# Performance work log

Hardware: AMD Instinct MI355X
Metric: run time of the kernel (lower is better)

The kernel has to match this reference:

```python
import jax, jax.numpy as jnp
import numpy as np
import math

D_MODEL = 1024
EPS = 1e-6  # RMSNorm epsilon


def setup_inputs() -> dict:
    key = jax.random.key(0)
    ks = jax.random.split(key, 9)
    d = D_MODEL
    B, T = 4, 4096
    s = 1.0 / math.sqrt(d)
    return {
        "x": jax.random.normal(ks[0], (B, T, d), dtype=jnp.float32),
        "w_key": jax.random.normal(ks[1], (2 * d, d), dtype=jnp.float32) * s,  # Linear(d, 2d, bias=False)
        "conv_w": jax.random.normal(ks[2], (d, 1, 3), dtype=jnp.float32) * (1.0 / math.sqrt(3)),  # depthwise k=3
        "conv_b": jax.random.normal(ks[3], (d,), dtype=jnp.float32) * 0.02,
        "w1": jax.random.normal(ks[4], (2 * d, d), dtype=jnp.float32) * s,  # Linear(d, 2d)
        "b1": jax.random.normal(ks[5], (2 * d,), dtype=jnp.float32) * 0.02,
        "w2": jax.random.normal(ks[6], (d, 2 * d), dtype=jnp.float32) * (1.0 / math.sqrt(2 * d)),  # Linear(2d, d)
        "b2": jax.random.normal(ks[7], (d,), dtype=jnp.float32) * 0.02,
        "norm_w": jnp.ones((d,), dtype=jnp.float32),
    }


def parallel_lerp_scan(theta, alpha):
    # h_t = lerp(h_{t-1}, theta_t, alpha_t) = (1-alpha_t)*h_{t-1} + alpha_t*theta_t
    # Linear recurrence h_t = a_t*h_{t-1} + b_t -> log-depth associative scan.
    a = 1.0 - alpha
    b = alpha * theta

    def combine(c1, c2):
        a1, b1 = c1
        a2, b2 = c2
        return (a2 * a1, a2 * b1 + b2)

    _, h = jax.lax.associative_scan(combine, (a, b), axis=1)
    return h


def rms_norm(x, w):
    var = jnp.mean(jnp.square(x), axis=-1, keepdims=True)
    return x * jax.lax.rsqrt(var + EPS) * w


def reference(x, w_key, conv_w, conv_b, w1, b1, w2, b2, norm_w):
    d = x.shape[-1]
    res = jnp.einsum('btd,ed->bte', x, w_key)  # [B,T,2D]
    theta, alpha = res[..., :d], res[..., d:]
    h = parallel_lerp_scan(jnp.tanh(theta) * math.pi, jax.nn.sigmoid(alpha))
    h = h.astype(x.dtype)
    # causal depthwise conv: left-pad (k-1)=2 zeros along time
    h_t = jnp.transpose(h, (0, 2, 1))  # [B,D,T]
    conv = jax.lax.conv_general_dilated(
        h_t, conv_w, window_strides=(1,), padding=[(2, 0)],
        feature_group_count=d, dimension_numbers=('NCH', 'OIH', 'NCH'))
    h_bound = jnp.transpose(conv + conv_b[None, :, None], (0, 2, 1))  # [B,T,D]
    z = h + h_bound
    hid = jax.nn.silu(jnp.einsum('btd,ed->bte', z, w1) + b1)
    h_final = jnp.einsum('bte,de->btd', hid, w2) + b2
    return rms_norm(h_final, norm_w)
```

## Files before the change

### kernel.cpp

```cpp
#include <hip/hip_runtime.h>

typedef unsigned short u16;
typedef unsigned int u32;
typedef __attribute__((ext_vector_type(8))) short short8;
typedef __attribute__((ext_vector_type(4))) float f32x4;

#define T_LEN 4096
#define BATCH 4
#define M_TOT (BATCH*T_LEN)
#define NCHUNK 32
#define CLEN 128

__device__ __forceinline__ u16 f2bf(float f){
  u32 u = __builtin_bit_cast(u32, f);
  u32 r = (u + 0x7FFFu + ((u >> 16) & 1u)) >> 16;
  return (u16)r;
}
__device__ __forceinline__ float sigmoid_(float v){ return 1.f/(1.f + __expf(-v)); }
__device__ __forceinline__ float tanh_pi_(float v){
  return 3.14159265358979323846f * (1.f - 2.f/(1.f + __expf(2.f*v)));
}

__global__ __launch_bounds__(256) void cvt_bf16_k(const float* __restrict__ in,
                                                  u16* __restrict__ out, int n4){
  int g = blockIdx.x*256 + threadIdx.x;
  if (g >= n4) return;
  float4 v = reinterpret_cast<const float4*>(in)[g];
  reinterpret_cast<ushort4*>(out)[g] =
      make_ushort4(f2bf(v.x), f2bf(v.y), f2bf(v.z), f2bf(v.w));
}


#define GBAR() do { __builtin_amdgcn_sched_barrier(0); __builtin_amdgcn_s_barrier(); \
                    __builtin_amdgcn_sched_barrier(0); } while(0)
#define WAITLGKM0() do { asm volatile("s_waitcnt lgkmcnt(0)" ::: "memory"); \
                         __builtin_amdgcn_sched_barrier(0); } while(0)
#define VMCNT(n) do { asm volatile("s_waitcnt vmcnt(" #n ")" ::: "memory"); \
                      __builtin_amdgcn_sched_barrier(0); } while(0)

#define STAGE(buf, ab, q, kt) do { \
  const u16* _s = ((ab) ? Bb : Ab) + (size_t)(q)*rowK64 + (size_t)(kt)*64; \
  __builtin_amdgcn_global_load_lds( \
    (const __attribute__((address_space(1))) void*)_s, \
    (__attribute__((address_space(3))) void*)(smem + (buf)*65536 + (ab)*32768 + (q)*8192 + stb), \
    16, 0, 0); \
} while(0)

#define LDA(buf, m, kk) (*(const short8*)(smem + (buf)*65536 + aRow + (m)*2048 + ((kk) ? csw1 : csw0)))
#define LDB(buf, n, kk) (*(const short8*)(smem + (buf)*65536 + 32768 + bRow + (n)*2048 + ((kk) ? csw1 : csw0)))

#define LOADB(buf) do { _Pragma("unroll") for (int n=0;n<4;n++){ \
    bfr0[n] = LDB(buf,n,0); bfr1[n] = LDB(buf,n,1); } } while(0)

#define PHASE_Q(buf, q, STMTS, ENDSTMT) do { \
  short8 _a00 = LDA(buf, 2*(q)  , 0); \
  short8 _a01 = LDA(buf, 2*(q)  , 1); \
  short8 _a10 = LDA(buf, 2*(q)+1, 0); \
  short8 _a11 = LDA(buf, 2*(q)+1, 1); \
  STMTS \
  GBAR(); \
  WAITLGKM0(); \
  __builtin_amdgcn_s_setprio(1); \
  _Pragma("unroll") \
  for (int n=0;n<4;n++){ \
    acc[2*(q)][n]   = __builtin_amdgcn_mfma_f32_16x16x32_bf16(_a00, bfr0[n], acc[2*(q)][n], 0,0,0); \
    acc[2*(q)][n]   = __builtin_amdgcn_mfma_f32_16x16x32_bf16(_a01, bfr1[n], acc[2*(q)][n], 0,0,0); \
    acc[2*(q)+1][n] = __builtin_amdgcn_mfma_f32_16x16x32_bf16(_a10, bfr0[n], acc[2*(q)+1][n], 0,0,0); \
    acc[2*(q)+1][n] = __builtin_amdgcn_mfma_f32_16x16x32_bf16(_a11, bfr1[n], acc[2*(q)+1][n], 0,0,0); \
  } \
  __builtin_amdgcn_s_setprio(0); \
  ENDSTMT \
  GBAR(); \
} while(0)

template<int EPI>
__global__ __launch_bounds__(512, 2) void gemm8p(
    const u16* __restrict__ Ag, const u16* __restrict__ Bg,
    const float* __restrict__ bias, void* __restrict__ Cout,
    int M, int N, int K)
{
  extern __shared__ __attribute__((aligned(16))) char smem[];
  const int tid = threadIdx.x;
  const int wid = tid >> 6, lane = tid & 63;
  const int wr = wid >> 2, wc = wid & 3;
  const int fr = lane & 15, fq = lane >> 4;

  const int nbn = N >> 8;
  const int nwg = gridDim.x;
  const int bid = blockIdx.x;
  const int swzb = (bid & 7) * (nwg >> 3) + (bid >> 3);
  const int bm = swzb / nbn, bn = swzb - bm * nbn;

  const size_t rowK64 = (size_t)64 * K;
  const u16* Ab = Ag + ((size_t)bm*256 + (tid>>3)) * K + ((tid & 7) ^ ((tid >> 3) & 7)) * 8;
  const u16* Bb = Bg + ((size_t)bn*256 + (tid>>3)) * K + ((tid & 7) ^ ((tid >> 3) & 7)) * 8;
  const u32 stb = (u32)(wid << 10);

  const u32 aRow = (u32)(wr*128 + fr) * 128;
  const u32 bRow = (u32)(wc*64  + fr) * 128;
  const u32 csw0 = (u32)((fq*16)      ^ ((fr & 7) << 4));
  const u32 csw1 = (u32)((64 + fq*16) ^ ((fr & 7) << 4));

  f32x4 acc[8][4];
#pragma unroll
  for (int m=0;m<8;m++)
#pragma unroll
    for (int n=0;n<4;n++) acc[m][n] = f32x4{0.f,0.f,0.f,0.f};

  short8 bfr0[4], bfr1[4];

  const int NT = K >> 6;

  STAGE(0,1,0,0); STAGE(0,1,1,0); STAGE(0,1,2,0); STAGE(0,1,3,0);
  STAGE(0,0,0,0); STAGE(0,0,1,0); STAGE(0,0,2,0); STAGE(0,0,3,0);
  STAGE(1,1,0,1); STAGE(1,1,1,1); STAGE(1,1,2,1); STAGE(1,1,3,1);
  STAGE(1,0,0,1); STAGE(1,0,2,1);
  VMCNT(6);
  GBAR();

  for (int i = 0; i < (NT>>1) - 1; ++i){
    const int tt = 2*i;
    PHASE_Q(0, 0, LOADB(0); STAGE(1,0,1,tt+1); STAGE(1,0,3,tt+1);, );
    PHASE_Q(0, 1, STAGE(0,1,0,tt+2); STAGE(0,1,1,tt+2);, );
    PHASE_Q(0, 2, STAGE(0,1,2,tt+2); STAGE(0,1,3,tt+2);, );
    PHASE_Q(0, 3, STAGE(0,0,0,tt+2); STAGE(0,0,2,tt+2);, VMCNT(6); );
    PHASE_Q(1, 0, LOADB(1); STAGE(0,0,1,tt+2); STAGE(0,0,3,tt+2);, );
    PHASE_Q(1, 1, STAGE(1,1,0,tt+3); STAGE(1,1,1,tt+3);, );
    PHASE_Q(1, 2, STAGE(1,1,2,tt+3); STAGE(1,1,3,tt+3);, );
    PHASE_Q(1, 3, STAGE(1,0,0,tt+3); STAGE(1,0,2,tt+3);, VMCNT(6); );
  }
  {
    const int tt = NT-2;
    PHASE_Q(0, 0, LOADB(0); STAGE(1,0,1,tt+1); STAGE(1,0,3,tt+1);, );
    PHASE_Q(0, 1, , );
    PHASE_Q(0, 2, , );
    PHASE_Q(0, 3, , VMCNT(0); );
    PHASE_Q(1, 0, LOADB(1);, );
    PHASE_Q(1, 1, , );
    PHASE_Q(1, 2, , );
    PHASE_Q(1, 3, , );
  }

  const int orow0 = bm*256 + wr*128;
  const int ocol0 = bn*256 + wc*64;
#pragma unroll
  for (int m=0;m<8;m++){
#pragma unroll
    for (int n=0;n<4;n++){
      const int col = ocol0 + n*16 + fr;
#pragma unroll
      for (int r=0;r<4;r++){
        const int row = orow0 + m*16 + fq*4 + r;
        float v = acc[m][n][r];
        if constexpr (EPI == 0){
          float o = (col < 1024) ? tanh_pi_(v) : sigmoid_(v);
          ((float*)Cout)[(size_t)row*N + col] = o;
        } else if constexpr (EPI == 1){
          v += bias[col];
          ((u16*)Cout)[(size_t)row*N + col] = f2bf(v * sigmoid_(v));
        } else {
          v += bias[col];
          ((float*)Cout)[(size_t)row*N + col] = v;
        }
      }
    }
  }
}

__global__ __launch_bounds__(256) void scan_stage1(const float* __restrict__ res,
                                                   float* __restrict__ sA,
                                                   float* __restrict__ sB){
  const int c     = (blockIdx.x & 3)*256 + threadIdx.x;
  const int chunk = (blockIdx.x >> 2) & (NCHUNK-1);
  const int b     = blockIdx.x >> 7;
  const float* p = res + ((size_t)(b*T_LEN + chunk*CLEN))*2048 + c;
  float A = 1.f, Bv = 0.f;
#pragma unroll 4
  for (int t=0;t<CLEN;++t){
    float th = p[0];
    float s  = p[1024];
    float a  = 1.f - s;
    A  *= a;
    Bv  = a*Bv + s*th;
    p  += 2048;
  }
  const int idx = (b*NCHUNK + chunk)*1024 + c;
  sA[idx] = A; sB[idx] = Bv;
}

__global__ __launch_bounds__(256) void scan_stage2(const float* __restrict__ sA,
                                                   const float* __restrict__ sB,
                                                   float* __restrict__ Hp){
  const int g = blockIdx.x*256 + threadIdx.x;
  const int b = g >> 10, c = g & 1023;
  float H = 0.f;
#pragma unroll
  for (int i=0;i<NCHUNK;++i){
    const int idx = (b*NCHUNK + i)*1024 + c;
    Hp[idx] = H;
    H = sA[idx]*H + sB[idx];
  }
}

__global__ __launch_bounds__(256) void scan_stage3(const float* __restrict__ res,
                                                   const float* __restrict__ Hp,
                                                   float* __restrict__ h){
  const int c     = (blockIdx.x & 3)*256 + threadIdx.x;
  const int chunk = (blockIdx.x >> 2) & (NCHUNK-1);
  const int b     = blockIdx.x >> 7;
  const float* p = res + ((size_t)(b*T_LEN + chunk*CLEN))*2048 + c;
  float*       q = h   + ((size_t)(b*T_LEN + chunk*CLEN))*1024 + c;
  float H = Hp[(b*NCHUNK + chunk)*1024 + c];
#pragma unroll 4
  for (int t=0;t<CLEN;++t){
    float th = p[0];
    float s  = p[1024];
    H = (1.f - s)*H + s*th;
    q[0] = H;
    p += 2048; q += 1024;
  }
}

__global__ __launch_bounds__(256) void conv_z_k(const float* __restrict__ h,
                                                const float* __restrict__ cw,
                                                const float* __restrict__ cb,
                                                u16* __restrict__ z){
  const int g = blockIdx.x*256 + threadIdx.x;
  const int c = g & 1023;
  const int t = (g >> 10) & (T_LEN-1);
  float h0  = h[g];
  float hm1 = (t >= 1) ? h[g-1024] : 0.f;
  float hm2 = (t >= 2) ? h[g-2048] : 0.f;
  float v = h0 + cb[c] + hm2*cw[3*c] + hm1*cw[3*c+1] + h0*cw[3*c+2];
  z[g] = f2bf(v);
}

__global__ __launch_bounds__(256) void rmsnorm_k(float* __restrict__ io,
                                                 const float* __restrict__ w){
  const int row = blockIdx.x;
  const int tid = threadIdx.x;
  float* p = io + (size_t)row*1024;
  float4 v = reinterpret_cast<const float4*>(p)[tid];
  float ss = v.x*v.x + v.y*v.y + v.z*v.z + v.w*v.w;
#pragma unroll
  for (int o=32; o>0; o>>=1) ss += __shfl_xor(ss, o, 64);
  __shared__ float red[4];
  if ((tid & 63) == 0) red[tid >> 6] = ss;
  __syncthreads();
  float tot = red[0] + red[1] + red[2] + red[3];
  float scale = rsqrtf(tot * (1.f/1024.f) + 1e-6f);
  float4 wv = reinterpret_cast<const float4*>(w)[tid];
  float4 o;
  o.x = v.x*scale*wv.x; o.y = v.y*scale*wv.y;
  o.z = v.z*scale*wv.z; o.w = v.w*scale*wv.w;
  reinterpret_cast<float4*>(p)[tid] = o;
}

extern "C" void kernel_launch(void* const* d_in, const int* in_sizes, int n_in,
                              void* d_out, int out_size, void* d_ws, size_t ws_size,
                              hipStream_t stream) {
  const float* x      = (const float*)d_in[0];
  const float* w_key  = (const float*)d_in[1];
  const float* conv_w = (const float*)d_in[2];
  const float* conv_b = (const float*)d_in[3];
  const float* w1     = (const float*)d_in[4];
  const float* b1     = (const float*)d_in[5];
  const float* w2     = (const float*)d_in[6];
  const float* b2     = (const float*)d_in[7];
  const float* norm_w = (const float*)d_in[8];
  float* out = (float*)d_out;
  char*  ws  = (char*)d_ws;

  size_t off = 0;
  float* RES  = (float*)(ws + off); off += (size_t)M_TOT*2048*4;
  float* HBUF = (float*)(ws + off); off += (size_t)M_TOT*1024*4;
  u16*   XB   = (u16*)  (ws + off); off += (size_t)M_TOT*1024*2;
  u16*   WK   = (u16*)  (ws + off); off += (size_t)2048*1024*2;
  u16*   W1B  = (u16*)  (ws + off); off += (size_t)2048*1024*2;
  u16*   W2B  = (u16*)  (ws + off); off += (size_t)1024*2048*2;
  float* SA   = (float*)(ws + off); off += (size_t)BATCH*NCHUNK*1024*4;
  float* SB   = (float*)(ws + off); off += (size_t)BATCH*NCHUNK*1024*4;
  float* HP   = (float*)(ws + off); off += (size_t)BATCH*NCHUNK*1024*4;
  u16* ZB  = XB;
  u16* HID = (u16*)RES;

  hipFuncSetAttribute((const void*)gemm8p<0>, hipFuncAttributeMaxDynamicSharedMemorySize, 131072);
  hipFuncSetAttribute((const void*)gemm8p<1>, hipFuncAttributeMaxDynamicSharedMemorySize, 131072);
  hipFuncSetAttribute((const void*)gemm8p<2>, hipFuncAttributeMaxDynamicSharedMemorySize, 131072);

  cvt_bf16_k<<<(M_TOT*1024/4 + 255)/256, 256, 0, stream>>>(x,     XB,  M_TOT*1024/4);
  cvt_bf16_k<<<(2048*1024/4  + 255)/256, 256, 0, stream>>>(w_key, WK,  2048*1024/4);
  cvt_bf16_k<<<(2048*1024/4  + 255)/256, 256, 0, stream>>>(w1,    W1B, 2048*1024/4);
  cvt_bf16_k<<<(1024*2048/4  + 255)/256, 256, 0, stream>>>(w2,    W2B, 1024*2048/4);

  gemm8p<0><<<(M_TOT/256)*(2048/256), 512, 131072, stream>>>(XB, WK, nullptr, RES, M_TOT, 2048, 1024);

  scan_stage1<<<BATCH*NCHUNK*4, 256, 0, stream>>>(RES, SA, SB);
  scan_stage2<<<16, 256, 0, stream>>>(SA, SB, HP);
  scan_stage3<<<BATCH*NCHUNK*4, 256, 0, stream>>>(RES, HP, HBUF);

  conv_z_k<<<(M_TOT*1024)/256, 256, 0, stream>>>(HBUF, conv_w, conv_b, ZB);

  gemm8p<1><<<(M_TOT/256)*(2048/256), 512, 131072, stream>>>(ZB, W1B, b1, HID, M_TOT, 2048, 1024);

  gemm8p<2><<<(M_TOT/256)*(1024/256), 512, 131072, stream>>>(HID, W2B, b2, out, M_TOT, 1024, 2048);

  rmsnorm_k<<<M_TOT, 256, 0, stream>>>(out, norm_w);
}
```

Measured before the change: 361.4 us.

## Fuse scan stage 3 with causal depthwise conv and relax GEMM sched barriers

```diff
diff --git a/kernel.cpp b/kernel.cpp
--- a/kernel.cpp
+++ b/kernel.cpp
@@ -31,12 +31,9 @@
 }
 
 
-#define GBAR() do { __builtin_amdgcn_sched_barrier(0); __builtin_amdgcn_s_barrier(); \
-                    __builtin_amdgcn_sched_barrier(0); } while(0)
-#define WAITLGKM0() do { asm volatile("s_waitcnt lgkmcnt(0)" ::: "memory"); \
-                         __builtin_amdgcn_sched_barrier(0); } while(0)
-#define VMCNT(n) do { asm volatile("s_waitcnt vmcnt(" #n ")" ::: "memory"); \
-                      __builtin_amdgcn_sched_barrier(0); } while(0)
+#define BAR() __builtin_amdgcn_s_barrier()
+#define WAITLGKM0() asm volatile("s_waitcnt lgkmcnt(0)" ::: "memory")
+#define VMCNT(n) asm volatile("s_waitcnt vmcnt(" #n ")" ::: "memory")
 
 #define STAGE(buf, ab, q, kt) do { \
   const u16* _s = ((ab) ? Bb : Ab) + (size_t)(q)*rowK64 + (size_t)(kt)*64; \
@@ -58,7 +55,7 @@
   short8 _a10 = LDA(buf, 2*(q)+1, 0); \
   short8 _a11 = LDA(buf, 2*(q)+1, 1); \
   STMTS \
-  GBAR(); \
+  BAR(); \
   WAITLGKM0(); \
   __builtin_amdgcn_s_setprio(1); \
   _Pragma("unroll") \
@@ -70,7 +67,7 @@
   } \
   __builtin_amdgcn_s_setprio(0); \
   ENDSTMT \
-  GBAR(); \
+  BAR(); \
 } while(0)
 
 template<int EPI>
@@ -116,7 +113,7 @@
   STAGE(1,1,0,1); STAGE(1,1,1,1); STAGE(1,1,2,1); STAGE(1,1,3,1);
   STAGE(1,0,0,1); STAGE(1,0,2,1);
   VMCNT(6);
-  GBAR();
+  BAR();
 
   for (int i = 0; i < (NT>>1) - 1; ++i){
     const int tt = 2*i;
@@ -169,14 +166,16 @@
 
 __global__ __launch_bounds__(256) void scan_stage1(const float* __restrict__ res,
                                                    float* __restrict__ sA,
-                                                   float* __restrict__ sB){
+                                                   float* __restrict__ sB,
+                                                   float* __restrict__ sA2,
+                                                   float* __restrict__ sB2){
   const int c     = (blockIdx.x & 3)*256 + threadIdx.x;
   const int chunk = (blockIdx.x >> 2) & (NCHUNK-1);
   const int b     = blockIdx.x >> 7;
   const float* p = res + ((size_t)(b*T_LEN + chunk*CLEN))*2048 + c;
   float A = 1.f, Bv = 0.f;
 #pragma unroll 4
-  for (int t=0;t<CLEN;++t){
+  for (int t=0;t<CLEN-1;++t){
     float th = p[0];
     float s  = p[1024];
     float a  = 1.f - s;
@@ -185,6 +184,14 @@
     p  += 2048;
   }
   const int idx = (b*NCHUNK + chunk)*1024 + c;
+  sA2[idx] = A; sB2[idx] = Bv;
+  {
+    float th = p[0];
+    float s  = p[1024];
+    float a  = 1.f - s;
+    A  *= a;
+    Bv  = a*Bv + s*th;
+  }
   sA[idx] = A; sB[idx] = Bv;
 }
 
@@ -202,37 +209,37 @@
   }
 }
 
-__global__ __launch_bounds__(256) void scan_stage3(const float* __restrict__ res,
-                                                   const float* __restrict__ Hp,
-                                                   float* __restrict__ h){
+__global__ __launch_bounds__(256) void scan3_conv_k(const float* __restrict__ res,
+                                                    const float* __restrict__ Hp,
+                                                    const float* __restrict__ sA2,
+                                                    const float* __restrict__ sB2,
+                                                    const float* __restrict__ cw,
+                                                    const float* __restrict__ cb,
+                                                    u16* __restrict__ z){
   const int c     = (blockIdx.x & 3)*256 + threadIdx.x;
   const int chunk = (blockIdx.x >> 2) & (NCHUNK-1);
   const int b     = blockIdx.x >> 7;
   const float* p = res + ((size_t)(b*T_LEN + chunk*CLEN))*2048 + c;
-  float*       q = h   + ((size_t)(b*T_LEN + chunk*CLEN))*1024 + c;
-  float H = Hp[(b*NCHUNK + chunk)*1024 + c];
+  u16*         q = z   + ((size_t)(b*T_LEN + chunk*CLEN))*1024 + c;
+  const int idx = (b*NCHUNK + chunk)*1024 + c;
+  float H   = Hp[idx];
+  float hm1 = H;
+  float hm2 = 0.f;
+  if (chunk > 0){
+    const int pidx = idx - 1024;
+    hm2 = sA2[pidx]*Hp[pidx] + sB2[pidx];
+  }
+  const float w0 = cw[3*c], w1 = cw[3*c+1], w2 = cw[3*c+2], bb = cb[c];
 #pragma unroll 4
   for (int t=0;t<CLEN;++t){
     float th = p[0];
     float s  = p[1024];
     H = (1.f - s)*H + s*th;
-    q[0] = H;
+    float v = H + bb + hm2*w0 + hm1*w1 + H*w2;
+    q[0] = f2bf(v);
+    hm2 = hm1; hm1 = H;
     p += 2048; q += 1024;
   }
-}
-
-__global__ __launch_bounds__(256) void conv_z_k(const float* __restrict__ h,
-                                                const float* __restrict__ cw,
-                                                const float* __restrict__ cb,
-                                                u16* __restrict__ z){
-  const int g = blockIdx.x*256 + threadIdx.x;
-  const int c = g & 1023;
-  const int t = (g >> 10) & (T_LEN-1);
-  float h0  = h[g];
-  float hm1 = (t >= 1) ? h[g-1024] : 0.f;
-  float hm2 = (t >= 2) ? h[g-2048] : 0.f;
-  float v = h0 + cb[c] + hm2*cw[3*c] + hm1*cw[3*c+1] + h0*cw[3*c+2];
-  z[g] = f2bf(v);
 }
 
 __global__ __launch_bounds__(256) void rmsnorm_k(float* __restrict__ io,
@@ -273,13 +280,14 @@
 
   size_t off = 0;
   float* RES  = (float*)(ws + off); off += (size_t)M_TOT*2048*4;
-  float* HBUF = (float*)(ws + off); off += (size_t)M_TOT*1024*4;
   u16*   XB   = (u16*)  (ws + off); off += (size_t)M_TOT*1024*2;
   u16*   WK   = (u16*)  (ws + off); off += (size_t)2048*1024*2;
   u16*   W1B  = (u16*)  (ws + off); off += (size_t)2048*1024*2;
   u16*   W2B  = (u16*)  (ws + off); off += (size_t)1024*2048*2;
   float* SA   = (float*)(ws + off); off += (size_t)BATCH*NCHUNK*1024*4;
   float* SB   = (float*)(ws + off); off += (size_t)BATCH*NCHUNK*1024*4;
+  float* SA2  = (float*)(ws + off); off += (size_t)BATCH*NCHUNK*1024*4;
+  float* SB2  = (float*)(ws + off); off += (size_t)BATCH*NCHUNK*1024*4;
   float* HP   = (float*)(ws + off); off += (size_t)BATCH*NCHUNK*1024*4;
   u16* ZB  = XB;
   u16* HID = (u16*)RES;
@@ -295,11 +303,9 @@
 
   gemm8p<0><<<(M_TOT/256)*(2048/256), 512, 131072, stream>>>(XB, WK, nullptr, RES, M_TOT, 2048, 1024);
 
-  scan_stage1<<<BATCH*NCHUNK*4, 256, 0, stream>>>(RES, SA, SB);
+  scan_stage1<<<BATCH*NCHUNK*4, 256, 0, stream>>>(RES, SA, SB, SA2, SB2);
   scan_stage2<<<16, 256, 0, stream>>>(SA, SB, HP);
-  scan_stage3<<<BATCH*NCHUNK*4, 256, 0, stream>>>(RES, HP, HBUF);
-
-  conv_z_k<<<(M_TOT*1024)/256, 256, 0, stream>>>(HBUF, conv_w, conv_b, ZB);
+  scan3_conv_k<<<BATCH*NCHUNK*4, 256, 0, stream>>>(RES, HP, SA2, SB2, conv_w, conv_b, ZB);
 
   gemm8p<1><<<(M_TOT/256)*(2048/256), 512, 131072, stream>>>(ZB, W1B, b1, HID, M_TOT, 2048, 1024);
 
```

New measurement: 328.8 us. 9.0% less time.
